# Optimization experiments

Hardware: AMD Instinct MI355X
Metric: run time of the kernel (lower is better)

Reference implementation:

```python
import jax, jax.numpy as jnp
import numpy as np

SCALE = 5.0          # smoothing scale (> 0 -> logsumexp smoothed min branch)
WINDOW = 16          # steps = interval[1] - interval[0] + 1 for interval [0, 15]
RNN_DIM = WINDOW - 1 # rnn_dim = interval[-1] = 15


def _minish(x, axis):
    # Minish.forward with scale > 0: -logsumexp(-x*scale, dim)/scale
    return -jax.nn.logsumexp(-x * SCALE, axis=axis) / SCALE


def _run(trace):
    # trace: [B, T, D]. Always._run_cell with bounded interval [0, 15].
    B, T, D = trace.shape
    # h0 = ones([B, rnn_dim, D]) * trace[:, :1, :]
    h0 = jnp.broadcast_to(trace[:, :1, :], (B, RNN_DIM, D))
    xs = jnp.swapaxes(trace, 0, 1)  # [T, B, D] for scan over time

    def step(h, x):
        # x: [B, D]; h: [B, RNN_DIM, D]
        # input = cat([h, x])[:, :steps] -> full 16-row window
        window = jnp.concatenate([h, x[:, None, :]], axis=1)  # [B, WINDOW, D]
        out = _minish(window, axis=1)                          # [B, D]
        # state = M @ h + b * x ; M is the k=1 shift matrix, b = e_last
        h_new = jnp.concatenate([h[:, 1:, :], x[:, None, :]], axis=1)
        return h_new, out

    _, outs = jax.lax.scan(step, h0, xs)   # outs: [T, B, D]
    return jnp.swapaxes(outs, 0, 1)        # [B, T, D]


def setup_inputs() -> dict:
    key = jax.random.key(0)
    k1, k2 = jax.random.split(key)
    B, T, D = 16, 8192, 64
    return {
        "lower_trace": jax.random.normal(k1, (B, T, D), dtype=jnp.float32),
        "upper_trace": jax.random.normal(k2, (B, T, D), dtype=jnp.float32),
    }


def reference(lower_trace, upper_trace):
    # subformula is identity; Always processes lower and upper bounds identically
    return _run(lower_trace), _run(upper_trace)
```

## Files before the change

### kernel.cpp

```cpp
#include <hip/hip_runtime.h>


#define TT     8192
#define DD     64
#define BB     16
#define LCH    16
#define CHUNKS (TT / LCH)

typedef float vfloat4 __attribute__((ext_vector_type(4)));

__device__ __forceinline__ float4 exp4n(float4 v) {
    float4 r;
    r.x = __expf(-5.0f * v.x);
    r.y = __expf(-5.0f * v.y);
    r.z = __expf(-5.0f * v.z);
    r.w = __expf(-5.0f * v.w);
    return r;
}
__device__ __forceinline__ float4 add4(float4 a, float4 b) {
    return make_float4(a.x + b.x, a.y + b.y, a.z + b.z, a.w + b.w);
}
__device__ __forceinline__ vfloat4 mlog4(float4 v) {
    vfloat4 r;
    r.x = -0.2f * __logf(v.x);
    r.y = -0.2f * __logf(v.y);
    r.z = -0.2f * __logf(v.z);
    r.w = -0.2f * __logf(v.w);
    return r;
}

__global__ __launch_bounds__(256, 3) void always_minish_v6(
    const float* __restrict__ lower,
    const float* __restrict__ upper,
    float* __restrict__ out)
{
    const int lane  = threadIdx.x & 63;
    const int wv    = (blockIdx.x << 2) | (threadIdx.x >> 6);
    const int dq    = lane & 15;
    const int sq    = lane >> 4;
    const int g     = wv >> 9;
    const int chunk = wv & (CHUNKS - 1);
    const int seq   = (g << 2) | sq;
    const int tr    = seq >> 4;
    const int b     = seq & 15;

    const float* __restrict__ src =
        (tr ? upper : lower) + (size_t)b * TT * DD + dq * 4;
    float* __restrict__ dst = out + (size_t)seq * TT * DD + dq * 4;

    const int t0 = chunk * LCH;

    float4 h[16], a[16];
    #pragma unroll
    for (int j = 0; j < 16; ++j) {
        int t = t0 - 16 + j;
        if (t < 0) t = 0;
        h[j] = *(const float4*)(src + (size_t)t * DD);
    }
    #pragma unroll
    for (int k = 0; k < 16; ++k)
        a[k] = *(const float4*)(src + (size_t)(t0 + k) * DD);

    __builtin_amdgcn_sched_barrier(0);

    #pragma unroll
    for (int j = 0; j < 16; ++j) h[j] = exp4n(h[j]);
    #pragma unroll
    for (int k = 0; k < 16; ++k) a[k] = exp4n(a[k]);

    #pragma unroll
    for (int j = 14; j >= 0; --j) h[j] = add4(h[j], h[j + 1]);

    float4 p = make_float4(0.f, 0.f, 0.f, 0.f);
    #pragma unroll
    for (int k = 0; k < 16; ++k) {
        p = add4(p, a[k]);
        const float4 w = (k < 15) ? add4(h[k + 1], p) : p;
        __builtin_nontemporal_store(mlog4(w),
                                    (vfloat4*)(dst + (size_t)(t0 + k) * DD));
    }
}

extern "C" void kernel_launch(void* const* d_in, const int* in_sizes, int n_in,
                              void* d_out, int out_size, void* d_ws, size_t ws_size,
                              hipStream_t stream)
{
    const float* lower = (const float*)d_in[0];
    const float* upper = (const float*)d_in[1];
    float* out = (float*)d_out;

    dim3 grid(1024), block(256);
    hipLaunchKernelGGL(always_minish_v6, grid, block, 0, stream,
                       lower, upper, out);
}
```

Baseline: 112.9 us.

## Process 64-step strips per wave with scalar lanes, reusing exp'd halo blocks

Each wave now handles one 64-timestep strip of a sequence, with one lane per feature, instead of a 16-step chunk with float4 lanes. Consecutive 16-step blocks reuse the previous block's exponentiated values as the halo, so the 16-row halo is loaded and exponentiated once per 64 outputs rather than once per 16. This cuts redundant loads and exp work. Loads of later blocks are interleaved with compute on earlier ones, and the occupancy hint is raised to 4. In exchange, memory accesses become 4-byte scalar per lane instead of 16-byte vectors, and each thread holds more registers.

```diff
diff --git a/kernel.cpp b/kernel.cpp
--- a/kernel.cpp
+++ b/kernel.cpp
@@ -3,82 +3,69 @@
 
 #define TT     8192
 #define DD     64
-#define BB     16
-#define LCH    16
-#define CHUNKS (TT / LCH)
+#define STRIPS 128
+#define SLEN   (TT / STRIPS)
 
-typedef float vfloat4 __attribute__((ext_vector_type(4)));
+#define BLOCK(PREV, CUR, tb)                                              \
+    {                                                                     \
+        _Pragma("unroll")                                                 \
+        for (int k = 0; k < 16; ++k) CUR[k] = __expf(-5.0f * CUR[k]);     \
+        _Pragma("unroll")                                                 \
+        for (int j = 14; j >= 0; --j) PREV[j] += PREV[j + 1];             \
+        float p = 0.f;                                                    \
+        _Pragma("unroll")                                                 \
+        for (int k = 0; k < 16; ++k) {                                    \
+            p += CUR[k];                                                  \
+            const float w = (k < 15) ? (PREV[k + 1] + p) : p;             \
+            __builtin_nontemporal_store(-0.2f * __logf(w),                \
+                dst + (size_t)((tb) + k) * DD);                           \
+        }                                                                 \
+    }
 
-__device__ __forceinline__ float4 exp4n(float4 v) {
-    float4 r;
-    r.x = __expf(-5.0f * v.x);
-    r.y = __expf(-5.0f * v.y);
-    r.z = __expf(-5.0f * v.z);
-    r.w = __expf(-5.0f * v.w);
-    return r;
-}
-__device__ __forceinline__ float4 add4(float4 a, float4 b) {
-    return make_float4(a.x + b.x, a.y + b.y, a.z + b.z, a.w + b.w);
-}
-__device__ __forceinline__ vfloat4 mlog4(float4 v) {
-    vfloat4 r;
-    r.x = -0.2f * __logf(v.x);
-    r.y = -0.2f * __logf(v.y);
-    r.z = -0.2f * __logf(v.z);
-    r.w = -0.2f * __logf(v.w);
-    return r;
-}
-
-__global__ __launch_bounds__(256, 3) void always_minish_v6(
+__global__ __launch_bounds__(256, 4) void always_minish_v8(
     const float* __restrict__ lower,
     const float* __restrict__ upper,
     float* __restrict__ out)
 {
     const int lane  = threadIdx.x & 63;
     const int wv    = (blockIdx.x << 2) | (threadIdx.x >> 6);
-    const int dq    = lane & 15;
-    const int sq    = lane >> 4;
-    const int g     = wv >> 9;
-    const int chunk = wv & (CHUNKS - 1);
-    const int seq   = (g << 2) | sq;
+    const int seq   = wv >> 7;
+    const int strip = wv & (STRIPS - 1);
     const int tr    = seq >> 4;
     const int b     = seq & 15;
 
     const float* __restrict__ src =
-        (tr ? upper : lower) + (size_t)b * TT * DD + dq * 4;
-    float* __restrict__ dst = out + (size_t)seq * TT * DD + dq * 4;
+        (tr ? upper : lower) + (size_t)b * TT * DD + lane;
+    float* __restrict__ dst = out + (size_t)seq * TT * DD + lane;
 
-    const int t0 = chunk * LCH;
+    const int t0 = strip * SLEN;
 
-    float4 h[16], a[16];
+    float H[16], X[16], Y[16], Z[16];
+
     #pragma unroll
     for (int j = 0; j < 16; ++j) {
         int t = t0 - 16 + j;
         if (t < 0) t = 0;
-        h[j] = *(const float4*)(src + (size_t)t * DD);
+        H[j] = src[(size_t)t * DD];
     }
     #pragma unroll
-    for (int k = 0; k < 16; ++k)
-        a[k] = *(const float4*)(src + (size_t)(t0 + k) * DD);
-
-    __builtin_amdgcn_sched_barrier(0);
+    for (int k = 0; k < 16; ++k) X[k] = src[(size_t)(t0 + k) * DD];
+    #pragma unroll
+    for (int k = 0; k < 16; ++k) Y[k] = src[(size_t)(t0 + 16 + k) * DD];
 
     #pragma unroll
-    for (int j = 0; j < 16; ++j) h[j] = exp4n(h[j]);
-    #pragma unroll
-    for (int k = 0; k < 16; ++k) a[k] = exp4n(a[k]);
+    for (int j = 0; j < 16; ++j) H[j] = __expf(-5.0f * H[j]);
 
     #pragma unroll
-    for (int j = 14; j >= 0; --j) h[j] = add4(h[j], h[j + 1]);
+    for (int k = 0; k < 16; ++k) Z[k] = src[(size_t)(t0 + 32 + k) * DD];
+    BLOCK(H, X, t0);
 
-    float4 p = make_float4(0.f, 0.f, 0.f, 0.f);
     #pragma unroll
-    for (int k = 0; k < 16; ++k) {
-        p = add4(p, a[k]);
-        const float4 w = (k < 15) ? add4(h[k + 1], p) : p;
-        __builtin_nontemporal_store(mlog4(w),
-                                    (vfloat4*)(dst + (size_t)(t0 + k) * DD));
-    }
+    for (int k = 0; k < 16; ++k) H[k] = src[(size_t)(t0 + 48 + k) * DD];
+    BLOCK(X, Y, t0 + 16);
+
+    BLOCK(Y, Z, t0 + 32);
+    BLOCK(Z, H, t0 + 48);
 }
 
 extern "C" void kernel_launch(void* const* d_in, const int* in_sizes, int n_in,
@@ -90,6 +77,6 @@
     float* out = (float*)d_out;
 
     dim3 grid(1024), block(256);
-    hipLaunchKernelGGL(always_minish_v6, grid, block, 0, stream,
+    hipLaunchKernelGGL(always_minish_v8, grid, block, 0, stream,
                        lower, upper, out);
 }
```

Measured after the change: 111.3 us. Within noise of the previous version (-1.4%).

## Split time across lanes with shuffle-based prefix sums over 64-step strips

Applied to the files above, without the earlier changes.

Each wave now handles one sequence over a 64-timestep strip, with the four lane groups each owning four consecutive timesteps. Cross-lane prefix and suffix sums of the exponentials are built with shuffles, and a carry is passed between 16-step blocks. This cuts the redundant 16-row halo reloads from one per 16 outputs to one per 64, and it prefetches the next block while the current one is being processed. The cost is cross-lane shuffle traffic, a longer serial dependency chain per wave, and an odd comma-expression load that relies on the compiler accepting it.

```diff
diff --git a/kernel.cpp b/kernel.cpp
--- a/kernel.cpp
+++ b/kernel.cpp
@@ -3,12 +3,14 @@
 
 #define TT     8192
 #define DD     64
-#define BB     16
-#define LCH    16
-#define CHUNKS (TT / LCH)
+#define STRIPS 128
+#define SLEN   (TT / STRIPS)
 
 typedef float vfloat4 __attribute__((ext_vector_type(4)));
 
+__device__ __forceinline__ float4 add4(float4 a, float4 b) {
+    return make_float4(a.x + b.x, a.y + b.y, a.z + b.z, a.w + b.w);
+}
 __device__ __forceinline__ float4 exp4n(float4 v) {
     float4 r;
     r.x = __expf(-5.0f * v.x);
@@ -16,9 +18,6 @@
     r.z = __expf(-5.0f * v.z);
     r.w = __expf(-5.0f * v.w);
     return r;
-}
-__device__ __forceinline__ float4 add4(float4 a, float4 b) {
-    return make_float4(a.x + b.x, a.y + b.y, a.z + b.z, a.w + b.w);
 }
 __device__ __forceinline__ vfloat4 mlog4(float4 v) {
     vfloat4 r;
@@ -28,57 +27,111 @@
     r.w = -0.2f * __logf(v.w);
     return r;
 }
+__device__ __forceinline__ float4 shflu(float4 v, int d) {
+    float4 r;
+    r.x = __shfl_up(v.x, d); r.y = __shfl_up(v.y, d);
+    r.z = __shfl_up(v.z, d); r.w = __shfl_up(v.w, d);
+    return r;
+}
+__device__ __forceinline__ float4 shfld(float4 v, int d) {
+    float4 r;
+    r.x = __shfl_down(v.x, d); r.y = __shfl_down(v.y, d);
+    r.z = __shfl_down(v.z, d); r.w = __shfl_down(v.w, d);
+    return r;
+}
+#define Z4 make_float4(0.f, 0.f, 0.f, 0.f)
 
-__global__ __launch_bounds__(256, 3) void always_minish_v6(
+struct Carry { float4 s[4]; };
+
+__device__ __forceinline__ void make_carry(const float4 R[4], int st, Carry& c) {
+    const float4 q3 = R[3];
+    const float4 q2 = add4(R[2], q3);
+    const float4 q1 = add4(R[1], q2);
+    const float4 q0 = add4(R[0], q1);
+    const float4 rc_raw = shfld(q0, 16);
+    const float4 rc = (st <= 2) ? rc_raw : Z4;
+    const float4 rd_raw = shfld(add4(rc, q0), 32);
+    const float4 rex = add4(rc, (st <= 1) ? rd_raw : Z4);
+    c.s[0] = add4(q1, rex);
+    c.s[1] = add4(q2, rex);
+    c.s[2] = add4(q3, rex);
+    const float4 rinc = add4(q0, rex);
+    const float4 c3_raw = shfld(rinc, 16);
+    c.s[3] = (st <= 2) ? c3_raw : Z4;
+}
+
+__device__ __forceinline__ void block_out(float4 R[4], Carry& c, int st,
+                                          float* __restrict__ dst, int tb) {
+    #pragma unroll
+    for (int k = 0; k < 4; ++k) R[k] = exp4n(R[k]);
+    const float4 p0 = R[0];
+    const float4 p1 = add4(p0, R[1]);
+    const float4 p2 = add4(p1, R[2]);
+    const float4 p3 = add4(p2, R[3]);
+    const float4 cu_raw = shflu(p3, 16);
+    const float4 cu = (st >= 1) ? cu_raw : Z4;
+    const float4 du_raw = shflu(add4(cu, p3), 32);
+    const float4 ex = add4(cu, (st >= 2) ? du_raw : Z4);
+    const float4 W0 = add4(c.s[0], add4(ex, p0));
+    const float4 W1 = add4(c.s[1], add4(ex, p1));
+    const float4 W2 = add4(c.s[2], add4(ex, p2));
+    const float4 W3 = add4(c.s[3], add4(ex, p3));
+    make_carry(R, st, c);
+    vfloat4* __restrict__ d0 = (vfloat4*)(dst + (size_t)(tb + 4 * st) * DD);
+    __builtin_nontemporal_store(mlog4(W0), d0);
+    __builtin_nontemporal_store(mlog4(W1), d0 + DD / 4);
+    __builtin_nontemporal_store(mlog4(W2), d0 + 2 * (DD / 4));
+    __builtin_nontemporal_store(mlog4(W3), d0 + 3 * (DD / 4));
+}
+
+__global__ __launch_bounds__(256, 4) void always_minish_v9(
     const float* __restrict__ lower,
     const float* __restrict__ upper,
     float* __restrict__ out)
 {
     const int lane  = threadIdx.x & 63;
+    const int dq    = lane & 15;
+    const int st    = lane >> 4;
     const int wv    = (blockIdx.x << 2) | (threadIdx.x >> 6);
-    const int dq    = lane & 15;
-    const int sq    = lane >> 4;
-    const int g     = wv >> 9;
-    const int chunk = wv & (CHUNKS - 1);
-    const int seq   = (g << 2) | sq;
+    const int seq   = wv >> 7;
+    const int strip = wv & (STRIPS - 1);
     const int tr    = seq >> 4;
     const int b     = seq & 15;
 
-    const float* __restrict__ src =
-        (tr ? upper : lower) + (size_t)b * TT * DD + dq * 4;
+    const float4* __restrict__ srcv =
+        (const float4*)((tr ? upper : lower) + (size_t)b * TT * DD) + dq;
     float* __restrict__ dst = out + (size_t)seq * TT * DD + dq * 4;
 
-    const int t0 = chunk * LCH;
+    const int t0 = strip * SLEN;
 
-    float4 h[16], a[16];
+    float4 A[4], B[4], C[4];
+    Carry c;
+
     #pragma unroll
-    for (int j = 0; j < 16; ++j) {
-        int t = t0 - 16 + j;
+    for (int k = 0; k < 4; ++k) {
+        int t = t0 - 16 + 4 * st + k;
         if (t < 0) t = 0;
-        h[j] = *(const float4*)(src + (size_t)t * DD);
+        A[k] = *((const float4*)((const float*)0 + 0) , &srcv[(size_t)t * (DD / 4)]);
     }
     #pragma unroll
-    for (int k = 0; k < 16; ++k)
-        a[k] = *(const float4*)(src + (size_t)(t0 + k) * DD);
-
-    __builtin_amdgcn_sched_barrier(0);
+    for (int k = 0; k < 4; ++k) B[k] = srcv[(size_t)(t0 + 4 * st + k) * (DD / 4)];
+    #pragma unroll
+    for (int k = 0; k < 4; ++k) C[k] = srcv[(size_t)(t0 + 16 + 4 * st + k) * (DD / 4)];
 
     #pragma unroll
-    for (int j = 0; j < 16; ++j) h[j] = exp4n(h[j]);
-    #pragma unroll
-    for (int k = 0; k < 16; ++k) a[k] = exp4n(a[k]);
+    for (int k = 0; k < 4; ++k) A[k] = exp4n(A[k]);
+    make_carry(A, st, c);
 
     #pragma unroll
-    for (int j = 14; j >= 0; --j) h[j] = add4(h[j], h[j + 1]);
+    for (int k = 0; k < 4; ++k) A[k] = srcv[(size_t)(t0 + 32 + 4 * st + k) * (DD / 4)];
+    block_out(B, c, st, dst, t0);
 
-    float4 p = make_float4(0.f, 0.f, 0.f, 0.f);
     #pragma unroll
-    for (int k = 0; k < 16; ++k) {
-        p = add4(p, a[k]);
-        const float4 w = (k < 15) ? add4(h[k + 1], p) : p;
-        __builtin_nontemporal_store(mlog4(w),
-                                    (vfloat4*)(dst + (size_t)(t0 + k) * DD));
-    }
+    for (int k = 0; k < 4; ++k) B[k] = srcv[(size_t)(t0 + 48 + 4 * st + k) * (DD / 4)];
+    block_out(C, c, st, dst, t0 + 16);
+
+    block_out(A, c, st, dst, t0 + 32);
+    block_out(B, c, st, dst, t0 + 48);
 }
 
 extern "C" void kernel_launch(void* const* d_in, const int* in_sizes, int n_in,
@@ -90,6 +143,6 @@
     float* out = (float*)d_out;
 
     dim3 grid(1024), block(256);
-    hipLaunchKernelGGL(always_minish_v6, grid, block, 0, stream,
+    hipLaunchKernelGGL(always_minish_v9, grid, block, 0, stream,
                        lower, upper, out);
 }
```

Measured after the change: 113.1 us. About the same (+0.2%).
